# Performance work log

Hardware: AMD Instinct MI355X
Metric: run time of the kernel (lower is better)

The kernel has to match this reference:

```python
import itertools
import jax, jax.numpy as jnp
import numpy as np

N_OBJECTS = 32
GRAPHLET_SIZE = 3
N_FILTERS = 16
REL_DIM = 16
BATCH = 32
N_GROUP_QUERIES = 512
BETA = 1.0

# static combinatorial groups: all C(32,3) = 4960 index triples
GROUP_IDX = jnp.asarray(
    np.array(list(itertools.combinations(range(N_OBJECTS), GRAPHLET_SIZE)), dtype=np.int32)
)  # (G, g)


def setup_inputs() -> dict:
    key = jax.random.key(0)
    k1, k2, k3 = jax.random.split(key, 3)
    inputs = jax.random.normal(k1, (BATCH, N_OBJECTS, N_OBJECTS, REL_DIM), dtype=jnp.float32)
    group_logits = jax.random.normal(k2, (N_GROUP_QUERIES, N_OBJECTS), dtype=jnp.float32)
    filters = jax.random.normal(k3, (N_FILTERS, GRAPHLET_SIZE, GRAPHLET_SIZE, REL_DIM), dtype=jnp.float32)
    return {"inputs": inputs, "group_logits": group_logits, "filters": filters}


def reference(inputs, group_logits, filters):
    idx = GROUP_IDX  # (G, g)
    # gather sub-relation tensors for every group in one fused advanced-index:
    # (B, G, g, g, D)
    sub_rel = inputs[:, idx[:, :, None], idx[:, None, :], :]
    # relational inner product with all filters: (B, G, F)
    rel_conv = jnp.einsum('bgijd,fijd->bgf', sub_rel, filters)
    # soft group weights
    sp = jax.nn.softplus(group_logits)            # (Gi, N)
    group_obj_w = sp[:, idx]                      # (Gi, G, g) -- gather along object axis
    group_w = jnp.prod(group_obj_w, axis=-1)      # (Gi, G)
    norm_w = jax.nn.softmax(BETA * group_w, axis=-1)  # (Gi, G)
    # contract over combinatorial groups: (B, Gi, F)
    out = jnp.einsum('bnr,gn->bgr', rel_conv, norm_w)
    return out
```

## Files before the change

### kernel.cpp

```cpp
#include <hip/hip_runtime.h>
#include <hip/hip_bf16.h>

#define N_OBJ   32
#define G_TOTAL 4960
#define NPAIR   496
#define KTOT    1600
#define SEG01   0
#define SEG02   496
#define SEG12   992
#define SEGD0   1488
#define SEGD1   1520
#define SEGD2   1552
#define N_FILT  16
#define REL_D   16
#define BATCH   32
#define NQ      512
#define ZSPLIT  5
#define KCH     320
#define NIT     10

typedef __attribute__((ext_vector_type(8))) short bf16x8;
typedef __attribute__((ext_vector_type(4))) float f32x4;

static __device__ inline unsigned short f2bf(float x) {
    union { float f; unsigned int u; } v; v.f = x;
    unsigned int r = v.u + 0x7fffu + ((v.u >> 16) & 1u);
    return (unsigned short)(r >> 16);
}
static __device__ inline void gload_lds16(const void* g, void* l) {
    __builtin_amdgcn_global_load_lds(
        (const __attribute__((address_space(1))) unsigned int*)g,
        (__attribute__((address_space(3))) unsigned int*)(unsigned int)(uintptr_t)l,
        16, 0, 0);
}
static __device__ inline int pbase(int x) { return (x * (63 - x)) >> 1; }
static __device__ inline void unrank2(int u, int& x, int& y) {
    for (x = 0; x < 31; x++) { int len = 31 - x; if (u < len) break; u -= len; }
    y = x + 1 + u;
}
static __device__ inline float dot16(float4 a0, float4 a1, float4 a2, float4 a3,
                                     const float* F) {
    float4 f0 = *(const float4*)(F);
    float4 f1 = *(const float4*)(F + 4);
    float4 f2 = *(const float4*)(F + 8);
    float4 f3 = *(const float4*)(F + 12);
    float d = a0.x * f0.x + a0.y * f0.y + a0.z * f0.z + a0.w * f0.w;
    d += a1.x * f1.x + a1.y * f1.y + a1.z * f1.z + a1.w * f1.w;
    d += a2.x * f2.x + a2.y * f2.y + a2.z * f2.z + a2.w * f2.w;
    d += a3.x * f3.x + a3.y * f3.y + a3.z * f3.z + a3.w * f3.w;
    return d;
}

__global__ __launch_bounds__(1024) void k_normw(const float* __restrict__ logits,
                                                unsigned short* __restrict__ Wp) {
    __shared__ float sp[32];
    __shared__ float red[8];
    __shared__ float Wf[KTOT];
    int t = threadIdx.x;
    int q = blockIdx.x;

    if (t < N_OBJ) {
        float x = logits[q * N_OBJ + t];
        float ex = __expf(x);
        sp[t] = (x > 15.f) ? x : __logf(1.f + ex);
    }
    __syncthreads();

#pragma unroll
    for (int rep = 0; rep < 2; rep++) {
        int idx = t + rep * 1024;
        if (idx < 3 * NPAIR) {
            int which = idx / NPAIR;
            int u = idx - which * NPAIR;
            int x, y; unrank2(u, x, y);
            float pxy = sp[x] * sp[y];
            float s = 0.f;
            if (which == 0) {
                for (int c = y + 1; c < 32; c++) s += __expf(pxy * sp[c]);
            } else if (which == 1) {
                for (int c = x + 1; c < y; c++)  s += __expf(pxy * sp[c]);
            } else {
                for (int c = 0; c < x; c++)      s += __expf(pxy * sp[c]);
            }
            Wf[which * NPAIR + u] = s;
        }
    }
    __syncthreads();

    if (t < 512) {
        float lsum = (t < NPAIR) ? Wf[t] : 0.f;
#pragma unroll
        for (int off = 32; off; off >>= 1) lsum += __shfl_down(lsum, off, 64);
        if ((t & 63) == 0) red[t >> 6] = lsum;
    } else if (t < 608) {
        int which = (t - 512) >> 5, idx = t & 31;
        float s = 0.f;
        if (which == 0) {
            int base = pbase(idx);
            for (int u = idx + 1; u < 32; u++) s += Wf[SEG01 + base + u - idx - 1];
            Wf[SEGD0 + idx] = s;
        } else if (which == 1) {
            for (int a2 = 0; a2 < idx; a2++) s += Wf[SEG01 + pbase(a2) + idx - a2 - 1];
            Wf[SEGD1 + idx] = s;
        } else {
            for (int b2 = 0; b2 < idx; b2++) s += Wf[SEG12 + pbase(b2) + idx - b2 - 1];
            Wf[SEGD2 + idx] = s;
        }
    } else if (t < 624) {
        Wf[1584 + (t - 608)] = 0.f;
    }
    __syncthreads();

    if (t < KTOT / 2) {
        float total = red[0] + red[1] + red[2] + red[3] +
                      red[4] + red[5] + red[6] + red[7];
        float inv = 1.f / total;
        unsigned int pk = (unsigned int)f2bf(Wf[2 * t] * inv) |
                          ((unsigned int)f2bf(Wf[2 * t + 1] * inv) << 16);
        ((unsigned int*)(Wp + (size_t)q * KTOT))[t] = pk;
    }
}

__global__ __launch_bounds__(256) void k_pc(const float* __restrict__ inputs,
                                            const float* __restrict__ filters,
                                            unsigned short* __restrict__ Bp) {
    __shared__ __align__(16) float flt[16 * 180];
    int t = threadIdx.x;
    int bid = blockIdx.x;
    int b = bid / 9, ch = bid - b * 9;
    for (int i = t; i < 576; i += 256) {
        int i4 = i * 4;
        int f = i4 / 144;
        int r = i4 - f * 144;
        *(float4*)&flt[f * 180 + (r >> 4) * 20 + (r & 15)] = *(const float4*)(filters + i4);
    }
    __syncthreads();

    int lane = t & 63, fq = t >> 6;
    int u = ch * 64 + lane;
    if (u < NPAIR) {
        int x, y; unrank2(u, x, y);
        const float4* rxy = (const float4*)(inputs + (((size_t)b * 32 + x) * 32 + y) * 16);
        const float4* ryx = (const float4*)(inputs + (((size_t)b * 32 + y) * 32 + x) * 16);
        float4 a0 = rxy[0], a1 = rxy[1], a2 = rxy[2], a3 = rxy[3];
        float4 c0 = ryx[0], c1 = ryx[1], c2 = ryx[2], c3 = ryx[3];
#pragma unroll
        for (int fi = 0; fi < 4; fi++) {
            const float* F = &flt[(fq * 4 + fi) * 180];
            float v01 = dot16(a0, a1, a2, a3, F + 1 * 20) + dot16(c0, c1, c2, c3, F + 3 * 20);
            float v02 = dot16(a0, a1, a2, a3, F + 2 * 20) + dot16(c0, c1, c2, c3, F + 6 * 20);
            float v12 = dot16(a0, a1, a2, a3, F + 5 * 20) + dot16(c0, c1, c2, c3, F + 7 * 20);
            size_t nrow = ((size_t)b * 16 + fq * 4 + fi) * KTOT;
            Bp[nrow + SEG01 + u] = f2bf(v01);
            Bp[nrow + SEG02 + u] = f2bf(v02);
            Bp[nrow + SEG12 + u] = f2bf(v12);
        }
    } else if (u < 528) {
        int x = u - NPAIR;
        const float4* rxx = (const float4*)(inputs + (((size_t)b * 32 + x) * 32 + x) * 16);
        float4 a0 = rxx[0], a1 = rxx[1], a2 = rxx[2], a3 = rxx[3];
#pragma unroll
        for (int fi = 0; fi < 4; fi++) {
            const float* F = &flt[(fq * 4 + fi) * 180];
            float v0 = dot16(a0, a1, a2, a3, F + 0 * 20);
            float v4 = dot16(a0, a1, a2, a3, F + 4 * 20);
            float v8 = dot16(a0, a1, a2, a3, F + 8 * 20);
            size_t nrow = ((size_t)b * 16 + fq * 4 + fi) * KTOT;
            Bp[nrow + SEGD0 + x] = f2bf(v0);
            Bp[nrow + SEGD1 + x] = f2bf(v4);
            Bp[nrow + SEGD2 + x] = f2bf(v8);
        }
    } else if (ch == 8 && lane >= 16 && lane < 32) {
        int col = lane - 16;
#pragma unroll
        for (int fi = 0; fi < 4; fi++)
            Bp[((size_t)b * 16 + fq * 4 + fi) * KTOT + 1584 + col] = 0;
    }
}

__global__ __launch_bounds__(256) void k_gemm(const unsigned short* __restrict__ A,
                                              const unsigned short* __restrict__ Bm,
                                              float* __restrict__ part) {
    __shared__ __align__(16) unsigned short As[2][64 * 32];
    __shared__ __align__(16) unsigned short Bs[2][64 * 32];
    int tid = threadIdx.x;
    int q0 = blockIdx.x * 64, n0 = blockIdx.y * 64, z = blockIdx.z;
    int k0 = z * KCH;
    int wave = tid >> 6, lane = tid & 63;
    int wm = wave & 1, wn = wave >> 1;
    int row16 = lane & 15, quad = lane >> 4;

    int srow = tid >> 2;
    int schunk = (tid & 3) ^ ((srow >> 1) & 3);
    const unsigned short* ga = A + (size_t)(q0 + srow) * KTOT + k0 + schunk * 8;
    const unsigned short* gb = Bm + (size_t)(n0 + srow) * KTOT + k0 + schunk * 8;
    char* lA = (char*)&As[0][0] + tid * 16;
    char* lB = (char*)&Bs[0][0] + tid * 16;

    f32x4 acc[2][2] = {};
    int fchunk = (quad ^ ((row16 >> 1) & 3)) * 8;

    gload_lds16(ga, lA);
    gload_lds16(gb, lB);
    for (int it = 0; it < NIT; ++it) {
        __syncthreads();
        if (it + 1 < NIT) {
            int nb = (it + 1) & 1;
            gload_lds16(ga + (it + 1) * 32, lA + nb * 64 * 32 * 2);
            gload_lds16(gb + (it + 1) * 32, lB + nb * 64 * 32 * 2);
        }
        int buf = it & 1;
        bf16x8 afr[2], bfr[2];
#pragma unroll
        for (int mi = 0; mi < 2; mi++)
            afr[mi] = *(const bf16x8*)&As[buf][(wm * 32 + mi * 16 + row16) * 32 + fchunk];
#pragma unroll
        for (int ni = 0; ni < 2; ni++)
            bfr[ni] = *(const bf16x8*)&Bs[buf][(wn * 32 + ni * 16 + row16) * 32 + fchunk];
#pragma unroll
        for (int mi = 0; mi < 2; mi++)
#pragma unroll
            for (int ni = 0; ni < 2; ni++)
                acc[mi][ni] = __builtin_amdgcn_mfma_f32_16x16x32_bf16(
                    afr[mi], bfr[ni], acc[mi][ni], 0, 0, 0);
    }

    float* pz = part + (size_t)z * (NQ * 512);
#pragma unroll
    for (int mi = 0; mi < 2; mi++)
#pragma unroll
        for (int ni = 0; ni < 2; ni++)
#pragma unroll
            for (int r = 0; r < 4; r++) {
                int q = q0 + wm * 32 + mi * 16 + quad * 4 + r;
                int n = n0 + wn * 32 + ni * 16 + row16;
                pz[q * 512 + n] = acc[mi][ni][r];
            }
}

__global__ __launch_bounds__(256) void k_reduce(const float* __restrict__ part,
                                                float* __restrict__ out) {
    int gid = blockIdx.x * 256 + threadIdx.x;
    int q = gid >> 7;
    int n = (gid & 127) * 4;
    float4 a = *(const float4*)(part + q * 512 + n);
#pragma unroll
    for (int zz = 1; zz < ZSPLIT; zz++) {
        float4 b4 = *(const float4*)(part + (size_t)zz * (NQ * 512) + q * 512 + n);
        a.x += b4.x; a.y += b4.y; a.z += b4.z; a.w += b4.w;
    }
    *(float4*)(out + (size_t)(n >> 4) * (NQ * REL_D) + q * 16 + (n & 15)) = a;
}

extern "C" void kernel_launch(void* const* d_in, const int* in_sizes, int n_in,
                              void* d_out, int out_size, void* d_ws, size_t ws_size,
                              hipStream_t stream) {
    const float* inputs  = (const float*)d_in[0];
    const float* logits  = (const float*)d_in[1];
    const float* filters = (const float*)d_in[2];
    float* out = (float*)d_out;

    char* ws = (char*)d_ws;
    unsigned short* Wp = (unsigned short*)ws;
    unsigned short* Bp = (unsigned short*)(ws + 1638400);
    float*          part = (float*)(ws + 3276800);

    k_normw<<<NQ, 1024, 0, stream>>>(logits, Wp);
    k_pc<<<288, 256, 0, stream>>>(inputs, filters, Bp);
    k_gemm<<<dim3(8, 8, ZSPLIT), 256, 0, stream>>>(Wp, Bp, part);
    k_reduce<<<NQ * 512 / 4 / 256, 256, 0, stream>>>(part, out);
}
```

Before: 81.86 us.

## Merge front kernels and fold split-K reduction into GEMM via atomic counter

Combines the softmax-weight kernel and the pair-convolution kernel into a single launch, using block-role dispatch with 1024-thread blocks that each cover four former pc blocks. It also removes the separate reduce kernel: each GEMM tile increments a per-tile semaphore, and the last z-slice block sums the partials and writes the output. This cuts two kernel launches and their inter-kernel gaps, at the cost of threadfence/atomic overhead and a serialized tail reduction inside one block per tile. The semaphore is zeroed by the front kernel each call.

```diff
diff --git a/kernel.cpp b/kernel.cpp
--- a/kernel.cpp
+++ b/kernel.cpp
@@ -51,138 +51,147 @@
     return d;
 }
 
-__global__ __launch_bounds__(1024) void k_normw(const float* __restrict__ logits,
-                                                unsigned short* __restrict__ Wp) {
-    __shared__ float sp[32];
-    __shared__ float red[8];
-    __shared__ float Wf[KTOT];
+__global__ __launch_bounds__(1024) void k_front(const float* __restrict__ logits,
+                                                const float* __restrict__ inputs,
+                                                const float* __restrict__ filters,
+                                                unsigned short* __restrict__ Wp,
+                                                unsigned short* __restrict__ Bp,
+                                                int* __restrict__ sem) {
+    __shared__ __align__(16) char smem[11648];
     int t = threadIdx.x;
-    int q = blockIdx.x;
-
-    if (t < N_OBJ) {
-        float x = logits[q * N_OBJ + t];
-        float ex = __expf(x);
-        sp[t] = (x > 15.f) ? x : __logf(1.f + ex);
-    }
-    __syncthreads();
-
-#pragma unroll
-    for (int rep = 0; rep < 2; rep++) {
-        int idx = t + rep * 1024;
-        if (idx < 3 * NPAIR) {
-            int which = idx / NPAIR;
-            int u = idx - which * NPAIR;
-            int x, y; unrank2(u, x, y);
-            float pxy = sp[x] * sp[y];
+    int role = blockIdx.x;
+
+    if (role < NQ) {
+        float* sp  = (float*)smem;
+        float* red = (float*)(smem + 128);
+        float* Wf  = (float*)(smem + 192);
+        int q = role;
+        if (t < N_OBJ) {
+            float x = logits[q * N_OBJ + t];
+            float ex = __expf(x);
+            sp[t] = (x > 15.f) ? x : __logf(1.f + ex);
+        }
+        __syncthreads();
+
+#pragma unroll
+        for (int rep = 0; rep < 2; rep++) {
+            int idx = t + rep * 1024;
+            if (idx < 3 * NPAIR) {
+                int which = idx / NPAIR;
+                int u = idx - which * NPAIR;
+                int x, y; unrank2(u, x, y);
+                float pxy = sp[x] * sp[y];
+                float s = 0.f;
+                if (which == 0) {
+                    for (int c = y + 1; c < 32; c++) s += __expf(pxy * sp[c]);
+                } else if (which == 1) {
+                    for (int c = x + 1; c < y; c++)  s += __expf(pxy * sp[c]);
+                } else {
+                    for (int c = 0; c < x; c++)      s += __expf(pxy * sp[c]);
+                }
+                Wf[which * NPAIR + u] = s;
+            }
+        }
+        __syncthreads();
+
+        if (t < 512) {
+            float lsum = (t < NPAIR) ? Wf[t] : 0.f;
+#pragma unroll
+            for (int off = 32; off; off >>= 1) lsum += __shfl_down(lsum, off, 64);
+            if ((t & 63) == 0) red[t >> 6] = lsum;
+        } else if (t < 608) {
+            int which = (t - 512) >> 5, idx = t & 31;
             float s = 0.f;
             if (which == 0) {
-                for (int c = y + 1; c < 32; c++) s += __expf(pxy * sp[c]);
+                int base = pbase(idx);
+                for (int u = idx + 1; u < 32; u++) s += Wf[SEG01 + base + u - idx - 1];
+                Wf[SEGD0 + idx] = s;
             } else if (which == 1) {
-                for (int c = x + 1; c < y; c++)  s += __expf(pxy * sp[c]);
+                for (int a2 = 0; a2 < idx; a2++) s += Wf[SEG01 + pbase(a2) + idx - a2 - 1];
+                Wf[SEGD1 + idx] = s;
             } else {
-                for (int c = 0; c < x; c++)      s += __expf(pxy * sp[c]);
-            }
-            Wf[which * NPAIR + u] = s;
-        }
-    }
-    __syncthreads();
-
-    if (t < 512) {
-        float lsum = (t < NPAIR) ? Wf[t] : 0.f;
-#pragma unroll
-        for (int off = 32; off; off >>= 1) lsum += __shfl_down(lsum, off, 64);
-        if ((t & 63) == 0) red[t >> 6] = lsum;
-    } else if (t < 608) {
-        int which = (t - 512) >> 5, idx = t & 31;
-        float s = 0.f;
-        if (which == 0) {
-            int base = pbase(idx);
-            for (int u = idx + 1; u < 32; u++) s += Wf[SEG01 + base + u - idx - 1];
-            Wf[SEGD0 + idx] = s;
-        } else if (which == 1) {
-            for (int a2 = 0; a2 < idx; a2++) s += Wf[SEG01 + pbase(a2) + idx - a2 - 1];
-            Wf[SEGD1 + idx] = s;
-        } else {
-            for (int b2 = 0; b2 < idx; b2++) s += Wf[SEG12 + pbase(b2) + idx - b2 - 1];
-            Wf[SEGD2 + idx] = s;
-        }
-    } else if (t < 624) {
-        Wf[1584 + (t - 608)] = 0.f;
-    }
-    __syncthreads();
-
-    if (t < KTOT / 2) {
-        float total = red[0] + red[1] + red[2] + red[3] +
-                      red[4] + red[5] + red[6] + red[7];
-        float inv = 1.f / total;
-        unsigned int pk = (unsigned int)f2bf(Wf[2 * t] * inv) |
-                          ((unsigned int)f2bf(Wf[2 * t + 1] * inv) << 16);
-        ((unsigned int*)(Wp + (size_t)q * KTOT))[t] = pk;
-    }
-}
-
-__global__ __launch_bounds__(256) void k_pc(const float* __restrict__ inputs,
-                                            const float* __restrict__ filters,
-                                            unsigned short* __restrict__ Bp) {
-    __shared__ __align__(16) float flt[16 * 180];
-    int t = threadIdx.x;
-    int bid = blockIdx.x;
-    int b = bid / 9, ch = bid - b * 9;
-    for (int i = t; i < 576; i += 256) {
-        int i4 = i * 4;
-        int f = i4 / 144;
-        int r = i4 - f * 144;
-        *(float4*)&flt[f * 180 + (r >> 4) * 20 + (r & 15)] = *(const float4*)(filters + i4);
-    }
-    __syncthreads();
-
-    int lane = t & 63, fq = t >> 6;
-    int u = ch * 64 + lane;
-    if (u < NPAIR) {
-        int x, y; unrank2(u, x, y);
-        const float4* rxy = (const float4*)(inputs + (((size_t)b * 32 + x) * 32 + y) * 16);
-        const float4* ryx = (const float4*)(inputs + (((size_t)b * 32 + y) * 32 + x) * 16);
-        float4 a0 = rxy[0], a1 = rxy[1], a2 = rxy[2], a3 = rxy[3];
-        float4 c0 = ryx[0], c1 = ryx[1], c2 = ryx[2], c3 = ryx[3];
-#pragma unroll
-        for (int fi = 0; fi < 4; fi++) {
-            const float* F = &flt[(fq * 4 + fi) * 180];
-            float v01 = dot16(a0, a1, a2, a3, F + 1 * 20) + dot16(c0, c1, c2, c3, F + 3 * 20);
-            float v02 = dot16(a0, a1, a2, a3, F + 2 * 20) + dot16(c0, c1, c2, c3, F + 6 * 20);
-            float v12 = dot16(a0, a1, a2, a3, F + 5 * 20) + dot16(c0, c1, c2, c3, F + 7 * 20);
-            size_t nrow = ((size_t)b * 16 + fq * 4 + fi) * KTOT;
-            Bp[nrow + SEG01 + u] = f2bf(v01);
-            Bp[nrow + SEG02 + u] = f2bf(v02);
-            Bp[nrow + SEG12 + u] = f2bf(v12);
-        }
-    } else if (u < 528) {
-        int x = u - NPAIR;
-        const float4* rxx = (const float4*)(inputs + (((size_t)b * 32 + x) * 32 + x) * 16);
-        float4 a0 = rxx[0], a1 = rxx[1], a2 = rxx[2], a3 = rxx[3];
-#pragma unroll
-        for (int fi = 0; fi < 4; fi++) {
-            const float* F = &flt[(fq * 4 + fi) * 180];
-            float v0 = dot16(a0, a1, a2, a3, F + 0 * 20);
-            float v4 = dot16(a0, a1, a2, a3, F + 4 * 20);
-            float v8 = dot16(a0, a1, a2, a3, F + 8 * 20);
-            size_t nrow = ((size_t)b * 16 + fq * 4 + fi) * KTOT;
-            Bp[nrow + SEGD0 + x] = f2bf(v0);
-            Bp[nrow + SEGD1 + x] = f2bf(v4);
-            Bp[nrow + SEGD2 + x] = f2bf(v8);
-        }
-    } else if (ch == 8 && lane >= 16 && lane < 32) {
-        int col = lane - 16;
-#pragma unroll
-        for (int fi = 0; fi < 4; fi++)
-            Bp[((size_t)b * 16 + fq * 4 + fi) * KTOT + 1584 + col] = 0;
+                for (int b2 = 0; b2 < idx; b2++) s += Wf[SEG12 + pbase(b2) + idx - b2 - 1];
+                Wf[SEGD2 + idx] = s;
+            }
+        } else if (t < 624) {
+            Wf[1584 + (t - 608)] = 0.f;
+        }
+        __syncthreads();
+
+        if (t < KTOT / 2) {
+            float total = red[0] + red[1] + red[2] + red[3] +
+                          red[4] + red[5] + red[6] + red[7];
+            float inv = 1.f / total;
+            unsigned int pk = (unsigned int)f2bf(Wf[2 * t] * inv) |
+                              ((unsigned int)f2bf(Wf[2 * t + 1] * inv) << 16);
+            ((unsigned int*)(Wp + (size_t)q * KTOT))[t] = pk;
+        }
+    } else {
+        float* flt = (float*)smem;
+        int role2 = role - NQ;
+        if (role2 == 0 && t < 64) sem[t] = 0;
+        if (t < 576) {
+            int i4 = t * 4;
+            int f = i4 / 144;
+            int r = i4 - f * 144;
+            *(float4*)&flt[f * 180 + (r >> 4) * 20 + (r & 15)] = *(const float4*)(filters + i4);
+        }
+        __syncthreads();
+
+        int oldbid = role2 * 4 + (t >> 8);
+        int tp = t & 255;
+        int b = oldbid / 9, ch = oldbid - b * 9;
+        int lane = tp & 63, fq = tp >> 6;
+        int u = ch * 64 + lane;
+        if (u < NPAIR) {
+            int x, y; unrank2(u, x, y);
+            const float4* rxy = (const float4*)(inputs + (((size_t)b * 32 + x) * 32 + y) * 16);
+            const float4* ryx = (const float4*)(inputs + (((size_t)b * 32 + y) * 32 + x) * 16);
+            float4 a0 = rxy[0], a1 = rxy[1], a2 = rxy[2], a3 = rxy[3];
+            float4 c0 = ryx[0], c1 = ryx[1], c2 = ryx[2], c3 = ryx[3];
+#pragma unroll
+            for (int fi = 0; fi < 4; fi++) {
+                const float* F = &flt[(fq * 4 + fi) * 180];
+                float v01 = dot16(a0, a1, a2, a3, F + 1 * 20) + dot16(c0, c1, c2, c3, F + 3 * 20);
+                float v02 = dot16(a0, a1, a2, a3, F + 2 * 20) + dot16(c0, c1, c2, c3, F + 6 * 20);
+                float v12 = dot16(a0, a1, a2, a3, F + 5 * 20) + dot16(c0, c1, c2, c3, F + 7 * 20);
+                size_t nrow = ((size_t)b * 16 + fq * 4 + fi) * KTOT;
+                Bp[nrow + SEG01 + u] = f2bf(v01);
+                Bp[nrow + SEG02 + u] = f2bf(v02);
+                Bp[nrow + SEG12 + u] = f2bf(v12);
+            }
+        } else if (u < 528) {
+            int x = u - NPAIR;
+            const float4* rxx = (const float4*)(inputs + (((size_t)b * 32 + x) * 32 + x) * 16);
+            float4 a0 = rxx[0], a1 = rxx[1], a2 = rxx[2], a3 = rxx[3];
+#pragma unroll
+            for (int fi = 0; fi < 4; fi++) {
+                const float* F = &flt[(fq * 4 + fi) * 180];
+                float v0 = dot16(a0, a1, a2, a3, F + 0 * 20);
+                float v4 = dot16(a0, a1, a2, a3, F + 4 * 20);
+                float v8 = dot16(a0, a1, a2, a3, F + 8 * 20);
+                size_t nrow = ((size_t)b * 16 + fq * 4 + fi) * KTOT;
+                Bp[nrow + SEGD0 + x] = f2bf(v0);
+                Bp[nrow + SEGD1 + x] = f2bf(v4);
+                Bp[nrow + SEGD2 + x] = f2bf(v8);
+            }
+        } else if (ch == 8 && lane >= 16 && lane < 32) {
+            int col = lane - 16;
+#pragma unroll
+            for (int fi = 0; fi < 4; fi++)
+                Bp[((size_t)b * 16 + fq * 4 + fi) * KTOT + 1584 + col] = 0;
+        }
     }
 }
 
 __global__ __launch_bounds__(256) void k_gemm(const unsigned short* __restrict__ A,
                                               const unsigned short* __restrict__ Bm,
-                                              float* __restrict__ part) {
+                                              float* __restrict__ part,
+                                              float* __restrict__ out,
+                                              int* __restrict__ sem) {
     __shared__ __align__(16) unsigned short As[2][64 * 32];
     __shared__ __align__(16) unsigned short Bs[2][64 * 32];
+    __shared__ int islast;
     int tid = threadIdx.x;
     int q0 = blockIdx.x * 64, n0 = blockIdx.y * 64, z = blockIdx.z;
     int k0 = z * KCH;
@@ -236,20 +245,31 @@
                 int n = n0 + wn * 32 + ni * 16 + row16;
                 pz[q * 512 + n] = acc[mi][ni][r];
             }
-}
-
-__global__ __launch_bounds__(256) void k_reduce(const float* __restrict__ part,
-                                                float* __restrict__ out) {
-    int gid = blockIdx.x * 256 + threadIdx.x;
-    int q = gid >> 7;
-    int n = (gid & 127) * 4;
-    float4 a = *(const float4*)(part + q * 512 + n);
-#pragma unroll
-    for (int zz = 1; zz < ZSPLIT; zz++) {
-        float4 b4 = *(const float4*)(part + (size_t)zz * (NQ * 512) + q * 512 + n);
-        a.x += b4.x; a.y += b4.y; a.z += b4.z; a.w += b4.w;
-    }
-    *(float4*)(out + (size_t)(n >> 4) * (NQ * REL_D) + q * 16 + (n & 15)) = a;
+
+    __syncthreads();
+    if (tid == 0) {
+        __threadfence();
+        int tileid = blockIdx.x * 8 + blockIdx.y;
+        islast = (atomicAdd(&sem[tileid], 1) == ZSPLIT - 1);
+        if (islast) __threadfence();
+    }
+    __syncthreads();
+    if (islast) {
+        int qr = tid >> 2, nc = tid & 3;
+        int q = q0 + qr;
+        float4 s0 = {0,0,0,0}, s1 = s0, s2 = s0, s3 = s0;
+#pragma unroll
+        for (int z2 = 0; z2 < ZSPLIT; z2++) {
+            const float4* p4 = (const float4*)(part + (size_t)z2 * (NQ * 512) + q * 512 + n0 + nc * 16);
+            float4 b0 = p4[0], b1 = p4[1], b2 = p4[2], b3 = p4[3];
+            s0.x += b0.x; s0.y += b0.y; s0.z += b0.z; s0.w += b0.w;
+            s1.x += b1.x; s1.y += b1.y; s1.z += b1.z; s1.w += b1.w;
+            s2.x += b2.x; s2.y += b2.y; s2.z += b2.z; s2.w += b2.w;
+            s3.x += b3.x; s3.y += b3.y; s3.z += b3.z; s3.w += b3.w;
+        }
+        float4* orow = (float4*)(out + (size_t)((n0 >> 4) + nc) * (NQ * REL_D) + q * 16);
+        orow[0] = s0; orow[1] = s1; orow[2] = s2; orow[3] = s3;
+    }
 }
 
 extern "C" void kernel_launch(void* const* d_in, const int* in_sizes, int n_in,
@@ -264,9 +284,8 @@
     unsigned short* Wp = (unsigned short*)ws;
     unsigned short* Bp = (unsigned short*)(ws + 1638400);
     float*          part = (float*)(ws + 3276800);
-
-    k_normw<<<NQ, 1024, 0, stream>>>(logits, Wp);
-    k_pc<<<288, 256, 0, stream>>>(inputs, filters, Bp);
-    k_gemm<<<dim3(8, 8, ZSPLIT), 256, 0, stream>>>(Wp, Bp, part);
-    k_reduce<<<NQ * 512 / 4 / 256, 256, 0, stream>>>(part, out);
-}
+    int*            sem  = (int*)(ws + 8519680);
+
+    k_front<<<NQ + 72, 1024, 0, stream>>>(logits, inputs, filters, Wp, Bp, sem);
+    k_gemm<<<dim3(8, 8, ZSPLIT), 256, 0, stream>>>(Wp, Bp, part, out, sem);
+}
```

Measured after the change: 92.95 us. 1.14x slower.

## Merge weight and conv prep kernels into one launch; double GEMM split-K

Applied to the files above, without the earlier changes.

Combines the softmax-weight kernel and the pair-convolution kernel into a single launch whose blocks pick a role by block index, with the conv blocks widened to 1024 threads covering four of the former blocks each. This removes one kernel launch and lets the two independent prep stages run concurrently. It also doubles the split-K factor of the GEMM and halves the K chunk, giving the GEMM more blocks. The cost is a larger partial-sum buffer and more work in the reduction. Partial writes must still fit the workspace.

```diff
diff --git a/kernel.cpp b/kernel.cpp
--- a/kernel.cpp
+++ b/kernel.cpp
@@ -15,9 +15,9 @@
 #define REL_D   16
 #define BATCH   32
 #define NQ      512
-#define ZSPLIT  5
-#define KCH     320
-#define NIT     10
+#define ZSPLIT  10
+#define KCH     160
+#define NIT     5
 
 typedef __attribute__((ext_vector_type(8))) short bf16x8;
 typedef __attribute__((ext_vector_type(4))) float f32x4;
@@ -51,130 +51,134 @@
     return d;
 }
 
-__global__ __launch_bounds__(1024) void k_normw(const float* __restrict__ logits,
-                                                unsigned short* __restrict__ Wp) {
-    __shared__ float sp[32];
-    __shared__ float red[8];
-    __shared__ float Wf[KTOT];
+__global__ __launch_bounds__(1024) void k_front(const float* __restrict__ logits,
+                                                const float* __restrict__ inputs,
+                                                const float* __restrict__ filters,
+                                                unsigned short* __restrict__ Wp,
+                                                unsigned short* __restrict__ Bp) {
+    __shared__ __align__(16) char smem[11648];
     int t = threadIdx.x;
-    int q = blockIdx.x;
-
-    if (t < N_OBJ) {
-        float x = logits[q * N_OBJ + t];
-        float ex = __expf(x);
-        sp[t] = (x > 15.f) ? x : __logf(1.f + ex);
-    }
-    __syncthreads();
-
-#pragma unroll
-    for (int rep = 0; rep < 2; rep++) {
-        int idx = t + rep * 1024;
-        if (idx < 3 * NPAIR) {
-            int which = idx / NPAIR;
-            int u = idx - which * NPAIR;
-            int x, y; unrank2(u, x, y);
-            float pxy = sp[x] * sp[y];
+    int role = blockIdx.x;
+
+    if (role < NQ) {
+        float* sp  = (float*)smem;
+        float* red = (float*)(smem + 128);
+        float* Wf  = (float*)(smem + 192);
+        int q = role;
+        if (t < N_OBJ) {
+            float x = logits[q * N_OBJ + t];
+            float ex = __expf(x);
+            sp[t] = (x > 15.f) ? x : __logf(1.f + ex);
+        }
+        __syncthreads();
+
+#pragma unroll
+        for (int rep = 0; rep < 2; rep++) {
+            int idx = t + rep * 1024;
+            if (idx < 3 * NPAIR) {
+                int which = idx / NPAIR;
+                int u = idx - which * NPAIR;
+                int x, y; unrank2(u, x, y);
+                float pxy = sp[x] * sp[y];
+                float s = 0.f;
+                if (which == 0) {
+                    for (int c = y + 1; c < 32; c++) s += __expf(pxy * sp[c]);
+                } else if (which == 1) {
+                    for (int c = x + 1; c < y; c++)  s += __expf(pxy * sp[c]);
+                } else {
+                    for (int c = 0; c < x; c++)      s += __expf(pxy * sp[c]);
+                }
+                Wf[which * NPAIR + u] = s;
+            }
+        }
+        __syncthreads();
+
+        if (t < 512) {
+            float lsum = (t < NPAIR) ? Wf[t] : 0.f;
+#pragma unroll
+            for (int off = 32; off; off >>= 1) lsum += __shfl_down(lsum, off, 64);
+            if ((t & 63) == 0) red[t >> 6] = lsum;
+        } else if (t < 608) {
+            int which = (t - 512) >> 5, idx = t & 31;
             float s = 0.f;
             if (which == 0) {
-                for (int c = y + 1; c < 32; c++) s += __expf(pxy * sp[c]);
+                int base = pbase(idx);
+                for (int u = idx + 1; u < 32; u++) s += Wf[SEG01 + base + u - idx - 1];
+                Wf[SEGD0 + idx] = s;
             } else if (which == 1) {
-                for (int c = x + 1; c < y; c++)  s += __expf(pxy * sp[c]);
+                for (int a2 = 0; a2 < idx; a2++) s += Wf[SEG01 + pbase(a2) + idx - a2 - 1];
+                Wf[SEGD1 + idx] = s;
             } else {
-                for (int c = 0; c < x; c++)      s += __expf(pxy * sp[c]);
-            }
-            Wf[which * NPAIR + u] = s;
-        }
-    }
-    __syncthreads();
-
-    if (t < 512) {
-        float lsum = (t < NPAIR) ? Wf[t] : 0.f;
-#pragma unroll
-        for (int off = 32; off; off >>= 1) lsum += __shfl_down(lsum, off, 64);
-        if ((t & 63) == 0) red[t >> 6] = lsum;
-    } else if (t < 608) {
-        int which = (t - 512) >> 5, idx = t & 31;
-        float s = 0.f;
-        if (which == 0) {
-            int base = pbase(idx);
-            for (int u = idx + 1; u < 32; u++) s += Wf[SEG01 + base + u - idx - 1];
-            Wf[SEGD0 + idx] = s;
-        } else if (which == 1) {
-            for (int a2 = 0; a2 < idx; a2++) s += Wf[SEG01 + pbase(a2) + idx - a2 - 1];
-            Wf[SEGD1 + idx] = s;
-        } else {
-            for (int b2 = 0; b2 < idx; b2++) s += Wf[SEG12 + pbase(b2) + idx - b2 - 1];
-            Wf[SEGD2 + idx] = s;
-        }
-    } else if (t < 624) {
-        Wf[1584 + (t - 608)] = 0.f;
-    }
-    __syncthreads();
-
-    if (t < KTOT / 2) {
-        float total = red[0] + red[1] + red[2] + red[3] +
-                      red[4] + red[5] + red[6] + red[7];
-        float inv = 1.f / total;
-        unsigned int pk = (unsigned int)f2bf(Wf[2 * t] * inv) |
-                          ((unsigned int)f2bf(Wf[2 * t + 1] * inv) << 16);
-        ((unsigned int*)(Wp + (size_t)q * KTOT))[t] = pk;
-    }
-}
-
-__global__ __launch_bounds__(256) void k_pc(const float* __restrict__ inputs,
-                                            const float* __restrict__ filters,
-                                            unsigned short* __restrict__ Bp) {
-    __shared__ __align__(16) float flt[16 * 180];
-    int t = threadIdx.x;
-    int bid = blockIdx.x;
-    int b = bid / 9, ch = bid - b * 9;
-    for (int i = t; i < 576; i += 256) {
-        int i4 = i * 4;
-        int f = i4 / 144;
-        int r = i4 - f * 144;
-        *(float4*)&flt[f * 180 + (r >> 4) * 20 + (r & 15)] = *(const float4*)(filters + i4);
-    }
-    __syncthreads();
-
-    int lane = t & 63, fq = t >> 6;
-    int u = ch * 64 + lane;
-    if (u < NPAIR) {
-        int x, y; unrank2(u, x, y);
-        const float4* rxy = (const float4*)(inputs + (((size_t)b * 32 + x) * 32 + y) * 16);
-        const float4* ryx = (const float4*)(inputs + (((size_t)b * 32 + y) * 32 + x) * 16);
-        float4 a0 = rxy[0], a1 = rxy[1], a2 = rxy[2], a3 = rxy[3];
-        float4 c0 = ryx[0], c1 = ryx[1], c2 = ryx[2], c3 = ryx[3];
-#pragma unroll
-        for (int fi = 0; fi < 4; fi++) {
-            const float* F = &flt[(fq * 4 + fi) * 180];
-            float v01 = dot16(a0, a1, a2, a3, F + 1 * 20) + dot16(c0, c1, c2, c3, F + 3 * 20);
-            float v02 = dot16(a0, a1, a2, a3, F + 2 * 20) + dot16(c0, c1, c2, c3, F + 6 * 20);
-            float v12 = dot16(a0, a1, a2, a3, F + 5 * 20) + dot16(c0, c1, c2, c3, F + 7 * 20);
-            size_t nrow = ((size_t)b * 16 + fq * 4 + fi) * KTOT;
-            Bp[nrow + SEG01 + u] = f2bf(v01);
-            Bp[nrow + SEG02 + u] = f2bf(v02);
-            Bp[nrow + SEG12 + u] = f2bf(v12);
-        }
-    } else if (u < 528) {
-        int x = u - NPAIR;
-        const float4* rxx = (const float4*)(inputs + (((size_t)b * 32 + x) * 32 + x) * 16);
-        float4 a0 = rxx[0], a1 = rxx[1], a2 = rxx[2], a3 = rxx[3];
-#pragma unroll
-        for (int fi = 0; fi < 4; fi++) {
-            const float* F = &flt[(fq * 4 + fi) * 180];
-            float v0 = dot16(a0, a1, a2, a3, F + 0 * 20);
-            float v4 = dot16(a0, a1, a2, a3, F + 4 * 20);
-            float v8 = dot16(a0, a1, a2, a3, F + 8 * 20);
-            size_t nrow = ((size_t)b * 16 + fq * 4 + fi) * KTOT;
-            Bp[nrow + SEGD0 + x] = f2bf(v0);
-            Bp[nrow + SEGD1 + x] = f2bf(v4);
-            Bp[nrow + SEGD2 + x] = f2bf(v8);
-        }
-    } else if (ch == 8 && lane >= 16 && lane < 32) {
-        int col = lane - 16;
-#pragma unroll
-        for (int fi = 0; fi < 4; fi++)
-            Bp[((size_t)b * 16 + fq * 4 + fi) * KTOT + 1584 + col] = 0;
+                for (int b2 = 0; b2 < idx; b2++) s += Wf[SEG12 + pbase(b2) + idx - b2 - 1];
+                Wf[SEGD2 + idx] = s;
+            }
+        } else if (t < 624) {
+            Wf[1584 + (t - 608)] = 0.f;
+        }
+        __syncthreads();
+
+        if (t < KTOT / 2) {
+            float total = red[0] + red[1] + red[2] + red[3] +
+                          red[4] + red[5] + red[6] + red[7];
+            float inv = 1.f / total;
+            unsigned int pk = (unsigned int)f2bf(Wf[2 * t] * inv) |
+                              ((unsigned int)f2bf(Wf[2 * t + 1] * inv) << 16);
+            ((unsigned int*)(Wp + (size_t)q * KTOT))[t] = pk;
+        }
+    } else {
+        float* flt = (float*)smem;
+        int role2 = role - NQ;
+        if (t < 576) {
+            int i4 = t * 4;
+            int f = i4 / 144;
+            int r = i4 - f * 144;
+            *(float4*)&flt[f * 180 + (r >> 4) * 20 + (r & 15)] = *(const float4*)(filters + i4);
+        }
+        __syncthreads();
+
+        int oldbid = role2 * 4 + (t >> 8);
+        int tp = t & 255;
+        int b = oldbid / 9, ch = oldbid - b * 9;
+        int lane = tp & 63, fq = tp >> 6;
+        int u = ch * 64 + lane;
+        if (u < NPAIR) {
+            int x, y; unrank2(u, x, y);
+            const float4* rxy = (const float4*)(inputs + (((size_t)b * 32 + x) * 32 + y) * 16);
+            const float4* ryx = (const float4*)(inputs + (((size_t)b * 32 + y) * 32 + x) * 16);
+            float4 a0 = rxy[0], a1 = rxy[1], a2 = rxy[2], a3 = rxy[3];
+            float4 c0 = ryx[0], c1 = ryx[1], c2 = ryx[2], c3 = ryx[3];
+#pragma unroll
+            for (int fi = 0; fi < 4; fi++) {
+                const float* F = &flt[(fq * 4 + fi) * 180];
+                float v01 = dot16(a0, a1, a2, a3, F + 1 * 20) + dot16(c0, c1, c2, c3, F + 3 * 20);
+                float v02 = dot16(a0, a1, a2, a3, F + 2 * 20) + dot16(c0, c1, c2, c3, F + 6 * 20);
+                float v12 = dot16(a0, a1, a2, a3, F + 5 * 20) + dot16(c0, c1, c2, c3, F + 7 * 20);
+                size_t nrow = ((size_t)b * 16 + fq * 4 + fi) * KTOT;
+                Bp[nrow + SEG01 + u] = f2bf(v01);
+                Bp[nrow + SEG02 + u] = f2bf(v02);
+                Bp[nrow + SEG12 + u] = f2bf(v12);
+            }
+        } else if (u < 528) {
+            int x = u - NPAIR;
+            const float4* rxx = (const float4*)(inputs + (((size_t)b * 32 + x) * 32 + x) * 16);
+            float4 a0 = rxx[0], a1 = rxx[1], a2 = rxx[2], a3 = rxx[3];
+#pragma unroll
+            for (int fi = 0; fi < 4; fi++) {
+                const float* F = &flt[(fq * 4 + fi) * 180];
+                float v0 = dot16(a0, a1, a2, a3, F + 0 * 20);
+                float v4 = dot16(a0, a1, a2, a3, F + 4 * 20);
+                float v8 = dot16(a0, a1, a2, a3, F + 8 * 20);
+                size_t nrow = ((size_t)b * 16 + fq * 4 + fi) * KTOT;
+                Bp[nrow + SEGD0 + x] = f2bf(v0);
+                Bp[nrow + SEGD1 + x] = f2bf(v4);
+                Bp[nrow + SEGD2 + x] = f2bf(v8);
+            }
+        } else if (ch == 8 && lane >= 16 && lane < 32) {
+            int col = lane - 16;
+#pragma unroll
+            for (int fi = 0; fi < 4; fi++)
+                Bp[((size_t)b * 16 + fq * 4 + fi) * KTOT + 1584 + col] = 0;
+        }
     }
 }
 
@@ -265,8 +269,7 @@
     unsigned short* Bp = (unsigned short*)(ws + 1638400);
     float*          part = (float*)(ws + 3276800);
 
-    k_normw<<<NQ, 1024, 0, stream>>>(logits, Wp);
-    k_pc<<<288, 256, 0, stream>>>(inputs, filters, Bp);
+    k_front<<<NQ + 72, 1024, 0, stream>>>(logits, inputs, filters, Wp, Bp);
     k_gemm<<<dim3(8, 8, ZSPLIT), 256, 0, stream>>>(Wp, Bp, part);
     k_reduce<<<NQ * 512 / 4 / 256, 256, 0, stream>>>(part, out);
 }
```

After: 81.15 us. Within noise of the previous version (-0.9%).
